# Optimization experiments

Hardware: AMD Instinct MI355X
Metric: run time of the kernel (lower is better)

Reference implementation:

```python
import jax, jax.numpy as jnp
import numpy as np

D_MODEL = 2048
N_HEADS = 16
D_HEAD = 128
INIT_RANGE = 0.02
EPSILON = -100000.0  # mask fill value from the original module


def setup_inputs() -> dict:
    key = jax.random.key(0)
    ks = jax.random.split(key, 6)
    x = jax.random.normal(ks[0], (2, 2048, D_MODEL), dtype=jnp.float32)
    W_Q = jax.random.normal(ks[1], (N_HEADS, D_MODEL, D_HEAD), dtype=jnp.float32) * INIT_RANGE
    W_K = jax.random.normal(ks[2], (N_HEADS, D_MODEL, D_HEAD), dtype=jnp.float32) * INIT_RANGE
    W_V = jax.random.normal(ks[3], (N_HEADS, D_MODEL, D_HEAD), dtype=jnp.float32) * INIT_RANGE
    W_O = jax.random.normal(ks[4], (N_HEADS, D_HEAD, D_MODEL), dtype=jnp.float32) * INIT_RANGE
    b_Q = jnp.zeros((N_HEADS, D_HEAD), dtype=jnp.float32)
    b_K = jnp.zeros((N_HEADS, D_HEAD), dtype=jnp.float32)
    b_V = jnp.zeros((N_HEADS, D_HEAD), dtype=jnp.float32)
    b_O = jnp.zeros((D_MODEL,), dtype=jnp.float32)
    return {"normalized_resid_pre": x, "W_Q": W_Q, "b_Q": b_Q, "W_K": W_K,
            "b_K": b_K, "W_V": W_V, "b_V": b_V, "W_O": W_O, "b_O": b_O}


def reference(normalized_resid_pre, W_Q, b_Q, W_K, b_K, W_V, b_V, W_O, b_O):
    x = normalized_resid_pre  # [b, s, d_model]
    # per-head projections: [b, s, h, d_head]
    q = jnp.einsum('bsd,hdk->bshk', x, W_Q) + b_Q
    k = jnp.einsum('bsd,hdk->bshk', x, W_K) + b_K
    v = jnp.einsum('bsd,hdk->bshk', x, W_V) + b_V
    # attention scores [b, h, q, k]
    scores = jnp.einsum('bqhk,bshk->bhqs', q, k) / jnp.sqrt(jnp.float32(D_HEAD))
    S = scores.shape[-1]
    causal = jnp.tril(jnp.ones((S, S), dtype=bool))  # True = keep
    scores = jnp.where(causal, scores, jnp.float32(EPSILON))
    pattern = jax.nn.softmax(scores, axis=-1)
    z = jnp.einsum('bhqs,bshk->bqhk', pattern, v)
    attn_out = jnp.einsum('bqhk,hkd->bqd', z, W_O) + b_O
    return attn_out
```

## Files before the change

### kernel.cpp

```cpp
#include <hip/hip_runtime.h>
#include <hip/hip_bf16.h>

typedef unsigned short bfu;
typedef short          bf16x8 __attribute__((ext_vector_type(8)));
typedef float          floatx4 __attribute__((ext_vector_type(4)));
typedef unsigned short bfu4 __attribute__((ext_vector_type(4)));
typedef unsigned int   u32x2 __attribute__((ext_vector_type(2)));

__device__ __forceinline__ bfu f2bf(float f) {
    __hip_bfloat16 h = __float2bfloat16(f);
    return __builtin_bit_cast(unsigned short, h);
}

__device__ __forceinline__ float ex2(float x) {
#if __has_builtin(__builtin_amdgcn_exp2f)
    return __builtin_amdgcn_exp2f(x);
#else
    return exp2f(x);
#endif
}

__device__ __forceinline__ void glds16(const bfu* g, bfu* l) {
    __builtin_amdgcn_global_load_lds(
        (const __attribute__((address_space(1))) unsigned int*)g,
        (__attribute__((address_space(3))) unsigned int*)l, 16, 0, 0);
}

#define BATCH 2
#define SEQ   2048
#define DM    2048
#define NH    16
#define DKH   128
#define SCALE  0.08838834764831845f
#define SCALEQ 0.1275174245f

__global__ __launch_bounds__(256)
void prep(const float* __restrict__ x, bfu* __restrict__ xb,
          const float* __restrict__ WQ, const float* __restrict__ WK,
          const float* __restrict__ WV,
          bfu* __restrict__ WtQ, bfu* __restrict__ WtK, bfu* __restrict__ WtV) {
    __shared__ float tile[64][65];
    const int bid = blockIdx.x;
    if (bid < 8192) {
        const int i = (bid * 256 + threadIdx.x) * 4;
        const float4 v = *(const float4*)(x + i);
        bfu4 p; p[0] = f2bf(v.x); p[1] = f2bf(v.y); p[2] = f2bf(v.z); p[3] = f2bf(v.w);
        *(bfu4*)(xb + i) = p;
        return;
    }
    const int idx = bid - 8192;
    const int gx = idx & 1, gy = (idx >> 1) & 31, gz = idx >> 6;
    const int p = gz >> 4, h = gz & 15;
    const float* src = ((p == 0) ? WQ : (p == 1) ? WK : WV) + (size_t)h * DM * DKH;
    bfu*         dst = ((p == 0) ? WtQ : (p == 1) ? WtK : WtV) + (size_t)h * DKH * DM;
    const float  s   = (p == 0) ? SCALEQ : 1.0f;
    const int r0 = gy * 64, c0 = gx * 64;
    const int t  = threadIdx.x;
    const int lr = t >> 4;
    const int lc = (t & 15) * 4;
    #pragma unroll
    for (int pp = 0; pp < 4; pp++) {
        const float4 v = *(const float4*)(src + (size_t)(r0 + pp*16 + lr) * DKH + c0 + lc);
        tile[pp*16 + lr][lc + 0] = v.x;
        tile[pp*16 + lr][lc + 1] = v.y;
        tile[pp*16 + lr][lc + 2] = v.z;
        tile[pp*16 + lr][lc + 3] = v.w;
    }
    __syncthreads();
    const int rc = t & 15, cb = t >> 4;
    #pragma unroll
    for (int pp = 0; pp < 4; pp++) {
        const int c = pp*16 + cb;
        bfu4 pk;
        #pragma unroll
        for (int j = 0; j < 4; j++) pk[j] = f2bf(tile[rc*4 + j][c] * s);
        *(bfu4*)(dst + (size_t)(c0 + c) * DM + r0 + rc*4) = pk;
    }
}

__global__ __launch_bounds__(256)
void tcvt_wo64(const float* __restrict__ WO, bfu* __restrict__ WtO) {
    __shared__ float tile[64][65];
    const int r0 = blockIdx.y * 64, c0 = blockIdx.x * 64;
    const int t  = threadIdx.x;
    const int lr = t >> 4;
    const int lc = (t & 15) * 4;
    #pragma unroll
    for (int pp = 0; pp < 4; pp++) {
        const float4 v = *(const float4*)(WO + (size_t)(r0 + pp*16 + lr) * DM + c0 + lc);
        tile[pp*16 + lr][lc + 0] = v.x;
        tile[pp*16 + lr][lc + 1] = v.y;
        tile[pp*16 + lr][lc + 2] = v.z;
        tile[pp*16 + lr][lc + 3] = v.w;
    }
    __syncthreads();
    const int rc = t & 15, cb = t >> 4;
    #pragma unroll
    for (int pp = 0; pp < 4; pp++) {
        const int c = pp*16 + cb;
        bfu4 pk;
        #pragma unroll
        for (int j = 0; j < 4; j++) pk[j] = f2bf(tile[rc*4 + j][c]);
        *(bfu4*)(WtO + (size_t)(c0 + c) * DM + r0 + rc*4) = pk;
    }
}

__device__ __forceinline__ void stg_half(const bfu* gbase, bfu* slot,
                                         int wave, int lane, int csw) {
    #pragma unroll
    for (int l = 0; l < 2; l++) {
        const int j = l * 8 + wave;
        glds16(gbase + (size_t)((j >> 1) * 16 + (lane >> 2)) * DM
                     + (j & 1) * 32 + csw,
               slot + j * 512);
    }
}

__device__ __forceinline__ void ld_b8(bf16x8 (&bv)[4][2], const bfu* slot, int rdo) {
    #pragma unroll
    for (int n = 0; n < 4; n++)
        #pragma unroll
        for (int ks = 0; ks < 2; ks++)
            bv[n][ks] = *(const bf16x8*)&slot[(n * 2 + ks) * 512 + rdo];
}

__device__ __forceinline__ void ld_a8(bf16x8 (&af)[4][2], const bfu* slot, int rdo) {
    #pragma unroll
    for (int m = 0; m < 4; m++)
        #pragma unroll
        for (int ks = 0; ks < 2; ks++)
            af[m][ks] = *(const bf16x8*)&slot[(m * 2 + ks) * 512 + rdo];
}

template<int MH, int NHALF>
__device__ __forceinline__ void mfma16(floatx4 (&acc)[8][4],
                                       const bf16x8 (&af)[4][2],
                                       const bf16x8 (&bv)[4][2]) {
    __builtin_amdgcn_s_setprio(1);
    #pragma unroll
    for (int m = 0; m < 4; m++)
        #pragma unroll
        for (int n = 0; n < 2; n++)
            #pragma unroll
            for (int ks = 0; ks < 2; ks++)
                acc[MH*4 + m][NHALF*2 + n] =
                    __builtin_amdgcn_mfma_f32_16x16x32_bf16(
                        af[m][ks], bv[NHALF*2 + n][ks],
                        acc[MH*4 + m][NHALF*2 + n], 0, 0, 0);
    __builtin_amdgcn_s_setprio(0);
}

#define BARW()                                                      \
    __builtin_amdgcn_s_barrier();                                   \
    asm volatile("s_waitcnt lgkmcnt(0)" ::: "memory");              \
    __builtin_amdgcn_sched_barrier(0)

__global__ __launch_bounds__(512, 2)
void proj_qk8(const bfu* __restrict__ xb,
              const bfu* __restrict__ WtQ, const bfu* __restrict__ WtK,
              const float* __restrict__ bQ, const float* __restrict__ bK,
              bfu* __restrict__ Qall, bfu* __restrict__ Kall) {
    __shared__ __align__(16) bfu As[2][2][8192];
    __shared__ __align__(16) bfu Bs[2][2][8192];

    const int p = blockIdx.y >> 3;
    const bfu*   Wt   = (p == 0) ? WtQ : WtK;
    const float* bias = (p == 0) ? bQ  : bK;
    const float  bscale = (p == 0) ? SCALEQ : 1.0f;

    const int tid  = threadIdx.x;
    const int lane = tid & 63;
    const int wave = tid >> 6;
    const int lrow = lane & 15;
    const int quad = lane >> 4;
    const int wr   = wave >> 2;
    const int wc   = wave & 3;
    const size_t m0 = (size_t)blockIdx.x * 256;
    const int    n0 = (int)(blockIdx.y & 7) * 256;

    const int csw = ((lane & 3) * 8) ^ ((lane & 32) ? 16 : 0);
    const int rdo = lrow * 32 + ((quad * 8) ^ ((lrow & 8) ? 16 : 0));

    const bfu* Ab = xb + m0 * DM;
    const bfu* Bb = Wt + (size_t)n0 * DM;

    floatx4 acc[8][4] = {};
    bf16x8 af[4][2], bv[4][2];

#define STAGE_A(tau, h)                                                     \
    if ((tau) < 32) stg_half(Ab + (size_t)((h) * 128) * DM + (tau) * 64,    \
                             &As[(tau) & 1][h][0], wave, lane, csw)
#define STAGE_B(tau, h)                                                     \
    if ((tau) < 32) stg_half(Bb + (size_t)((h) * 128) * DM + (tau) * 64,    \
                             &Bs[(tau) & 1][h][0], wave, lane, csw)

    STAGE_B(0, 0); STAGE_B(0, 1); STAGE_A(0, 0); STAGE_A(0, 1);
    STAGE_B(1, 0); STAGE_B(1, 1); STAGE_A(1, 0);
    asm volatile("s_waitcnt vmcnt(6)" ::: "memory");
    __builtin_amdgcn_s_barrier();

    #pragma unroll 1
    for (int i = 0; i < 16; i++) {
        const int t0 = 2 * i;
        ld_b8(bv, &Bs[0][wc >> 1][(wc & 1) * 4096], rdo);
        ld_a8(af, &As[0][wr][0], rdo);
        STAGE_A(t0 + 1, 1);
        BARW();
        mfma16<0, 0>(acc, af, bv);
        __builtin_amdgcn_s_barrier();
        STAGE_B(t0 + 2, 0);
        BARW();
        mfma16<0, 1>(acc, af, bv);
        __builtin_amdgcn_s_barrier();
        ld_a8(af, &As[0][wr][4096], rdo);
        STAGE_B(t0 + 2, 1);
        BARW();
        mfma16<1, 0>(acc, af, bv);
        __builtin_amdgcn_s_barrier();
        STAGE_A(t0 + 2, 0);
        BARW();
        mfma16<1, 1>(acc, af, bv);
        if (i == 15) asm volatile("s_waitcnt vmcnt(0)" ::: "memory");
        else         asm volatile("s_waitcnt vmcnt(6)" ::: "memory");
        __builtin_amdgcn_s_barrier();
        ld_b8(bv, &Bs[1][wc >> 1][(wc & 1) * 4096], rdo);
        ld_a8(af, &As[1][wr][0], rdo);
        STAGE_A(t0 + 2, 1);
        BARW();
        mfma16<0, 0>(acc, af, bv);
        __builtin_amdgcn_s_barrier();
        STAGE_B(t0 + 3, 0);
        BARW();
        mfma16<0, 1>(acc, af, bv);
        __builtin_amdgcn_s_barrier();
        ld_a8(af, &As[1][wr][4096], rdo);
        STAGE_B(t0 + 3, 1);
        BARW();
        mfma16<1, 0>(acc, af, bv);
        __builtin_amdgcn_s_barrier();
        STAGE_A(t0 + 3, 0);
        BARW();
        mfma16<1, 1>(acc, af, bv);
        if (i < 15) asm volatile("s_waitcnt vmcnt(6)" ::: "memory");
        __builtin_amdgcn_s_barrier();
    }
#undef STAGE_A
#undef STAGE_B

    bfu* Out = (p == 0) ? Qall : Kall;
    #pragma unroll
    for (int m = 0; m < 8; m++) {
        #pragma unroll
        for (int n = 0; n < 4; n++) {
            const int gn = n0 + wc * 64 + n * 16 + lrow;
            const float bvv = bias[gn] * bscale;
            #pragma unroll
            for (int r = 0; r < 4; r++) {
                const size_t gm = m0 + wr * 128 + m * 16 + quad * 4 + r;
                Out[gm * DM + gn] = f2bf(acc[m][n][r] + bvv);
            }
        }
    }
}

__global__ __launch_bounds__(256)
void proj_v(const bfu* __restrict__ xb, const bfu* __restrict__ WtV,
            const float* __restrict__ bV, bfu* __restrict__ Vt) {
    __shared__ bfu As[128 * 32];
    __shared__ bfu Bs[128 * 32];
    const int tid  = threadIdx.x;
    const int lane = tid & 63;
    const int wave = tid >> 6;
    const int lrow = lane & 15;
    const int quad = lane >> 4;
    const int mw = (wave & 1) * 64;
    const int nw = (wave >> 1) * 64;
    const size_t m0 = (size_t)blockIdx.x * 128;
    const size_t n0 = (size_t)blockIdx.y * 128;
    const int rowb = lane >> 2;
    const int colb = (lane & 3) * 8;

    floatx4 acc[4][4] = {};

    for (int k0 = 0; k0 < DM; k0 += 32) {
        __syncthreads();
        #pragma unroll
        for (int i = 0; i < 2; i++) {
            const int rg = wave * 2 + i;
            glds16(xb  + (m0 + rg*16 + rowb) * DM + k0 + colb, &As[rg * 512]);
            glds16(WtV + (n0 + rg*16 + rowb) * DM + k0 + colb, &Bs[rg * 512]);
        }
        __syncthreads();
        bf16x8 af[4], bfr[4];
        #pragma unroll
        for (int t = 0; t < 4; t++) {
            af[t]  = *(const bf16x8*)&As[(mw + t*16 + lrow) * 32 + quad * 8];
            bfr[t] = *(const bf16x8*)&Bs[(nw + t*16 + lrow) * 32 + quad * 8];
        }
        #pragma unroll
        for (int mt = 0; mt < 4; mt++)
            #pragma unroll
            for (int nt = 0; nt < 4; nt++)
                acc[mt][nt] = __builtin_amdgcn_mfma_f32_16x16x32_bf16(
                                  af[mt], bfr[nt], acc[mt][nt], 0, 0, 0);
    }

    #pragma unroll
    for (int mt = 0; mt < 4; mt++) {
        #pragma unroll
        for (int nt = 0; nt < 4; nt++) {
            const int nl = (int)n0 + nw + nt*16 + lrow;
            const float bvv = bV[nl];
            const size_t gm0 = m0 + mw + mt*16 + quad*4;
            const int b = (int)(gm0 >> 11), s = (int)(gm0 & 2047);
            bfu4 pk;
            #pragma unroll
            for (int r = 0; r < 4; r++) pk[r] = f2bf(acc[mt][nt][r] + bvv);
            *(bfu4*)&Vt[((size_t)(b * NH + (nl >> 7)) * DKH + (nl & 127)) * SEQ + s] = pk;
        }
    }
}

__global__ __launch_bounds__(256)
void flash_attn(const bfu* __restrict__ Q, const bfu* __restrict__ K,
                const bfu* __restrict__ Vt, bfu* __restrict__ Z) {
    __shared__ bfu Ks[4][64][32];
    __shared__ bfu Vs[2][128][32];
    __shared__ bfu Ps[4][16][72];

    const int tid  = threadIdx.x;
    const int lane = tid & 63;
    const int wave = tid >> 6;
    const int lrow = lane & 15;
    const int quad = lane >> 4;
    const int hb = blockIdx.x;
    const int h = hb & 15, b = hb >> 4;
    const int qt = 31 - blockIdx.y;
    const int q0w = qt * 64 + wave * 16;
    const int rowb = lane >> 2;
    const int csw  = ((lane & 3) * 8) ^ ((lane & 32) ? 16 : 0);
    const int rq0  = (quad * 8) ^ ((lrow & 8) ? 16 : 0);

    const bfu* Qrow = Q + (size_t)(b * SEQ + q0w + lrow) * DM + h * DKH;
    bf16x8 qf[4];
    #pragma unroll
    for (int kc = 0; kc < 4; kc++)
        qf[kc] = *(const bf16x8*)(Qrow + kc*32 + quad*8);

    floatx4 z[8] = {};
    float l_loc = 0.f;
    const int qg = q0w + lrow;

    const bfu* Kb = K + (size_t)b * SEQ * DM + h * DKH;
    const bfu* Vb = Vt + (size_t)(b * NH + h) * DKH * SEQ;
    const int ntiles = qt + 1;

    for (int it = 0; it < ntiles; it++) {
        const int s0 = it * 64;
        __syncthreads();
        #pragma unroll
        for (int i = 0; i < 8; i++) {
            const int chunk = wave * 8 + i;
            if (chunk < 16) {
                const int kc = chunk >> 2, kg = chunk & 3;
                glds16(Kb + (size_t)(s0 + kg*16 + rowb) * DM + kc*32 + csw,
                       &Ks[kc][kg*16][0]);
            } else {
                const int c2 = chunk - 16;
                const int sh = c2 >> 3, dg = c2 & 7;
                glds16(Vb + (size_t)(dg*16 + rowb) * SEQ + s0 + sh*32 + csw,
                       &Vs[sh][dg*16][0]);
            }
        }
        __syncthreads();

        floatx4 sc[4];
        __builtin_amdgcn_s_setprio(1);
        #pragma unroll
        for (int st = 0; st < 4; st++) {
            floatx4 a = {};
            #pragma unroll
            for (int kc = 0; kc < 4; kc++) {
                bf16x8 kf = *(const bf16x8*)&Ks[kc][st*16 + lrow][rq0];
                a = __builtin_amdgcn_mfma_f32_16x16x32_bf16(kf, qf[kc], a, 0, 0, 0);
            }
            sc[st] = a;
        }
        __builtin_amdgcn_s_setprio(0);

        if (it + 1 < ntiles) {
            #pragma unroll
            for (int st = 0; st < 4; st++) {
                const float p0 = ex2(sc[st][0]);
                const float p1 = ex2(sc[st][1]);
                const float p2 = ex2(sc[st][2]);
                const float p3 = ex2(sc[st][3]);
                l_loc += (p0 + p1) + (p2 + p3);
                u32x2 pk;
                pk[0] = (unsigned)f2bf(p0) | ((unsigned)f2bf(p1) << 16);
                pk[1] = (unsigned)f2bf(p2) | ((unsigned)f2bf(p3) << 16);
                *(u32x2*)&Ps[wave][lrow][st*16 + quad*4] = pk;
            }
        } else {
            #pragma unroll
            for (int st = 0; st < 4; st++) {
                const int sbase = s0 + st*16 + quad*4;
                const float p0 = (sbase + 0 <= qg) ? ex2(sc[st][0]) : 0.f;
                const float p1 = (sbase + 1 <= qg) ? ex2(sc[st][1]) : 0.f;
                const float p2 = (sbase + 2 <= qg) ? ex2(sc[st][2]) : 0.f;
                const float p3 = (sbase + 3 <= qg) ? ex2(sc[st][3]) : 0.f;
                l_loc += (p0 + p1) + (p2 + p3);
                u32x2 pk;
                pk[0] = (unsigned)f2bf(p0) | ((unsigned)f2bf(p1) << 16);
                pk[1] = (unsigned)f2bf(p2) | ((unsigned)f2bf(p3) << 16);
                *(u32x2*)&Ps[wave][lrow][st*16 + quad*4] = pk;
            }
        }

        bf16x8 pf0 = *(const bf16x8*)&Ps[wave][lrow][quad*8];
        bf16x8 pf1 = *(const bf16x8*)&Ps[wave][lrow][32 + quad*8];
        __builtin_amdgcn_s_setprio(1);
        #pragma unroll
        for (int dt = 0; dt < 8; dt++) {
            bf16x8 v0 = *(const bf16x8*)&Vs[0][dt*16 + lrow][rq0];
            z[dt] = __builtin_amdgcn_mfma_f32_16x16x32_bf16(pf0, v0, z[dt], 0, 0, 0);
            bf16x8 v1 = *(const bf16x8*)&Vs[1][dt*16 + lrow][rq0];
            z[dt] = __builtin_amdgcn_mfma_f32_16x16x32_bf16(pf1, v1, z[dt], 0, 0, 0);
        }
        __builtin_amdgcn_s_setprio(0);
    }

    float L = l_loc;
    L += __shfl_xor(L, 16);
    L += __shfl_xor(L, 32);
    float inv[4];
    #pragma unroll
    for (int r = 0; r < 4; r++)
        inv[r] = 1.0f / __shfl(L, quad*4 + r, 64);
    #pragma unroll
    for (int dt = 0; dt < 8; dt++) {
        #pragma unroll
        for (int r = 0; r < 4; r++) {
            const int qq = q0w + quad*4 + r;
            const int dk = dt*16 + lrow;
            Z[(size_t)(b * SEQ + qq) * DM + h * DKH + dk] = f2bf(z[dt][r] * inv[r]);
        }
    }
}

__global__ __launch_bounds__(256)
void out_gemm(const bfu* __restrict__ Zb, const bfu* __restrict__ WtO,
              const float* __restrict__ bO, float* out) {
    __shared__ bfu As[128 * 32];
    __shared__ bfu Bs[128 * 32];
    const int tid  = threadIdx.x;
    const int lane = tid & 63;
    const int wave = tid >> 6;
    const int lrow = lane & 15;
    const int quad = lane >> 4;
    const int mw = (wave & 1) * 64;
    const int nw = (wave >> 1) * 64;
    const size_t m0 = (size_t)blockIdx.x * 128;
    const size_t n0 = (size_t)blockIdx.y * 128;
    const int rowb = lane >> 2, colb = (lane & 3) * 8;

    floatx4 acc[4][4] = {};

    for (int k0 = 0; k0 < DM; k0 += 32) {
        __syncthreads();
        #pragma unroll
        for (int i = 0; i < 2; i++) {
            const int rg = wave * 2 + i;
            glds16(Zb  + (m0 + rg*16 + rowb) * DM + k0 + colb, &As[rg * 512]);
            glds16(WtO + (n0 + rg*16 + rowb) * DM + k0 + colb, &Bs[rg * 512]);
        }
        __syncthreads();
        bf16x8 af[4], bfr[4];
        #pragma unroll
        for (int t = 0; t < 4; t++) {
            af[t]  = *(const bf16x8*)&As[(mw + t*16 + lrow) * 32 + quad * 8];
            bfr[t] = *(const bf16x8*)&Bs[(nw + t*16 + lrow) * 32 + quad * 8];
        }
        #pragma unroll
        for (int mt = 0; mt < 4; mt++)
            #pragma unroll
            for (int nt = 0; nt < 4; nt++)
                acc[mt][nt] = __builtin_amdgcn_mfma_f32_16x16x32_bf16(
                                  af[mt], bfr[nt], acc[mt][nt], 0, 0, 0);
    }

    #pragma unroll
    for (int mt = 0; mt < 4; mt++) {
        #pragma unroll
        for (int nt = 0; nt < 4; nt++) {
            const size_t gn = n0 + nw + nt*16 + lrow;
            const float bv = bO[gn];
            #pragma unroll
            for (int r = 0; r < 4; r++) {
                const size_t gm = m0 + mw + mt*16 + quad*4 + r;
                out[gm * DM + gn] = acc[mt][nt][r] + bv;
            }
        }
    }
}

extern "C" void kernel_launch(void* const* d_in, const int* in_sizes, int n_in,
                              void* d_out, int out_size, void* d_ws, size_t ws_size,
                              hipStream_t stream) {
    const float* x  = (const float*)d_in[0];
    const float* WQ = (const float*)d_in[1];
    const float* bQ = (const float*)d_in[2];
    const float* WK = (const float*)d_in[3];
    const float* bK = (const float*)d_in[4];
    const float* WV = (const float*)d_in[5];
    const float* bV = (const float*)d_in[6];
    const float* WO = (const float*)d_in[7];
    const float* bO = (const float*)d_in[8];
    float* out = (float*)d_out;
    bfu* ws  = (bfu*)d_ws;
    bfu* dob = (bfu*)d_out;

    bfu* Qall = ws;
    bfu* Kall = Qall + 8388608;
    bfu* Vt   = Kall + 8388608;
    bfu* Zb   = Vt   + 8388608;
    bfu* WtV  = Zb;
    bfu* xb   = dob;
    bfu* WtQ  = dob + 8388608;
    bfu* WtK  = dob + 12582912;

    prep<<<11264, 256, 0, stream>>>(x, xb, WQ, WK, WV, WtQ, WtK, WtV);

    proj_qk8<<<dim3(16, 16), 512, 0, stream>>>(xb, WtQ, WtK, bQ, bK, Qall, Kall);
    proj_v<<<dim3(32, 16), 256, 0, stream>>>(xb, WtV, bV, Vt);

    flash_attn<<<dim3(32, 32), 256, 0, stream>>>(Qall, Kall, Vt, Zb);

    tcvt_wo64<<<dim3(32, 32), 256, 0, stream>>>(WO, Qall);
    out_gemm<<<dim3(32, 16), 256, 0, stream>>>(Zb, Qall, bO, out);
}
```

Before: 364.5 us.

## Double query rows per wave in flash attention to reuse K/V tiles

Each wave now handles 32 query rows (two 16-row MFMA tiles) and each block covers 128 queries, so the grid in the query dimension is halved. Each K/V tile loaded into LDS feeds twice as many MFMAs, which cuts global and LDS traffic per unit of work. Waves whose rows are fully masked for a tile skip compute with a continue after the barrier. The cost is more registers for the extra accumulators, fewer blocks, and more load imbalance from the causal mask across waves.

```diff
diff --git a/kernel.cpp b/kernel.cpp
--- a/kernel.cpp
+++ b/kernel.cpp
@@ -326,7 +326,7 @@
                 const bfu* __restrict__ Vt, bfu* __restrict__ Z) {
     __shared__ bfu Ks[4][64][32];
     __shared__ bfu Vs[2][128][32];
-    __shared__ bfu Ps[4][16][72];
+    __shared__ bfu Ps[4][32][72];
 
     const int tid  = threadIdx.x;
     const int lane = tid & 63;
@@ -335,25 +335,29 @@
     const int quad = lane >> 4;
     const int hb = blockIdx.x;
     const int h = hb & 15, b = hb >> 4;
-    const int qt = 31 - blockIdx.y;
-    const int q0w = qt * 64 + wave * 16;
+    const int qt = 15 - blockIdx.y;
+    const int q0w = qt * 128 + wave * 32;
     const int rowb = lane >> 2;
     const int csw  = ((lane & 3) * 8) ^ ((lane & 32) ? 16 : 0);
     const int rq0  = (quad * 8) ^ ((lrow & 8) ? 16 : 0);
 
-    const bfu* Qrow = Q + (size_t)(b * SEQ + q0w + lrow) * DM + h * DKH;
-    bf16x8 qf[4];
-    #pragma unroll
-    for (int kc = 0; kc < 4; kc++)
-        qf[kc] = *(const bf16x8*)(Qrow + kc*32 + quad*8);
-
-    floatx4 z[8] = {};
-    float l_loc = 0.f;
-    const int qg = q0w + lrow;
+    const bfu* Qrow0 = Q + (size_t)(b * SEQ + q0w + lrow) * DM + h * DKH;
+    const bfu* Qrow1 = Qrow0 + (size_t)16 * DM;
+    bf16x8 qf0[4], qf1[4];
+    #pragma unroll
+    for (int kc = 0; kc < 4; kc++) {
+        qf0[kc] = *(const bf16x8*)(Qrow0 + kc*32 + quad*8);
+        qf1[kc] = *(const bf16x8*)(Qrow1 + kc*32 + quad*8);
+    }
+
+    floatx4 z0[8] = {}, z1[8] = {};
+    float l0 = 0.f, l1 = 0.f;
+    const int qg0 = q0w + lrow;
+    const int qg1 = q0w + 16 + lrow;
 
     const bfu* Kb = K + (size_t)b * SEQ * DM + h * DKH;
     const bfu* Vb = Vt + (size_t)(b * NH + h) * DKH * SEQ;
-    const int ntiles = qt + 1;
+    const int ntiles = 2 * (qt + 1);
 
     for (int it = 0; it < ntiles; it++) {
         const int s0 = it * 64;
@@ -374,76 +378,106 @@
         }
         __syncthreads();
 
-        floatx4 sc[4];
+        if (s0 > q0w + 31) continue;
+
+        floatx4 sc0[4], sc1[4];
         __builtin_amdgcn_s_setprio(1);
         #pragma unroll
         for (int st = 0; st < 4; st++) {
-            floatx4 a = {};
+            floatx4 a0 = {}, a1 = {};
             #pragma unroll
             for (int kc = 0; kc < 4; kc++) {
                 bf16x8 kf = *(const bf16x8*)&Ks[kc][st*16 + lrow][rq0];
-                a = __builtin_amdgcn_mfma_f32_16x16x32_bf16(kf, qf[kc], a, 0, 0, 0);
+                a0 = __builtin_amdgcn_mfma_f32_16x16x32_bf16(kf, qf0[kc], a0, 0, 0, 0);
+                a1 = __builtin_amdgcn_mfma_f32_16x16x32_bf16(kf, qf1[kc], a1, 0, 0, 0);
             }
-            sc[st] = a;
+            sc0[st] = a0;
+            sc1[st] = a1;
         }
         __builtin_amdgcn_s_setprio(0);
 
-        if (it + 1 < ntiles) {
+        if (s0 + 64 <= q0w) {
             #pragma unroll
             for (int st = 0; st < 4; st++) {
-                const float p0 = ex2(sc[st][0]);
-                const float p1 = ex2(sc[st][1]);
-                const float p2 = ex2(sc[st][2]);
-                const float p3 = ex2(sc[st][3]);
-                l_loc += (p0 + p1) + (p2 + p3);
+                const float p0 = ex2(sc0[st][0]);
+                const float p1 = ex2(sc0[st][1]);
+                const float p2 = ex2(sc0[st][2]);
+                const float p3 = ex2(sc0[st][3]);
+                l0 += (p0 + p1) + (p2 + p3);
                 u32x2 pk;
                 pk[0] = (unsigned)f2bf(p0) | ((unsigned)f2bf(p1) << 16);
                 pk[1] = (unsigned)f2bf(p2) | ((unsigned)f2bf(p3) << 16);
                 *(u32x2*)&Ps[wave][lrow][st*16 + quad*4] = pk;
+                const float q0_ = ex2(sc1[st][0]);
+                const float q1_ = ex2(sc1[st][1]);
+                const float q2_ = ex2(sc1[st][2]);
+                const float q3_ = ex2(sc1[st][3]);
+                l1 += (q0_ + q1_) + (q2_ + q3_);
+                u32x2 qk;
+                qk[0] = (unsigned)f2bf(q0_) | ((unsigned)f2bf(q1_) << 16);
+                qk[1] = (unsigned)f2bf(q2_) | ((unsigned)f2bf(q3_) << 16);
+                *(u32x2*)&Ps[wave][16 + lrow][st*16 + quad*4] = qk;
             }
         } else {
             #pragma unroll
             for (int st = 0; st < 4; st++) {
                 const int sbase = s0 + st*16 + quad*4;
-                const float p0 = (sbase + 0 <= qg) ? ex2(sc[st][0]) : 0.f;
-                const float p1 = (sbase + 1 <= qg) ? ex2(sc[st][1]) : 0.f;
-                const float p2 = (sbase + 2 <= qg) ? ex2(sc[st][2]) : 0.f;
-                const float p3 = (sbase + 3 <= qg) ? ex2(sc[st][3]) : 0.f;
-                l_loc += (p0 + p1) + (p2 + p3);
+                const float p0 = (sbase + 0 <= qg0) ? ex2(sc0[st][0]) : 0.f;
+                const float p1 = (sbase + 1 <= qg0) ? ex2(sc0[st][1]) : 0.f;
+                const float p2 = (sbase + 2 <= qg0) ? ex2(sc0[st][2]) : 0.f;
+                const float p3 = (sbase + 3 <= qg0) ? ex2(sc0[st][3]) : 0.f;
+                l0 += (p0 + p1) + (p2 + p3);
                 u32x2 pk;
                 pk[0] = (unsigned)f2bf(p0) | ((unsigned)f2bf(p1) << 16);
                 pk[1] = (unsigned)f2bf(p2) | ((unsigned)f2bf(p3) << 16);
                 *(u32x2*)&Ps[wave][lrow][st*16 + quad*4] = pk;
+                const float q0_ = (sbase + 0 <= qg1) ? ex2(sc1[st][0]) : 0.f;
+                const float q1_ = (sbase + 1 <= qg1) ? ex2(sc1[st][1]) : 0.f;
+                const float q2_ = (sbase + 2 <= qg1) ? ex2(sc1[st][2]) : 0.f;
+                const float q3_ = (sbase + 3 <= qg1) ? ex2(sc1[st][3]) : 0.f;
+                l1 += (q0_ + q1_) + (q2_ + q3_);
+                u32x2 qk;
+                qk[0] = (unsigned)f2bf(q0_) | ((unsigned)f2bf(q1_) << 16);
+                qk[1] = (unsigned)f2bf(q2_) | ((unsigned)f2bf(q3_) << 16);
+                *(u32x2*)&Ps[wave][16 + lrow][st*16 + quad*4] = qk;
             }
         }
 
-        bf16x8 pf0 = *(const bf16x8*)&Ps[wave][lrow][quad*8];
-        bf16x8 pf1 = *(const bf16x8*)&Ps[wave][lrow][32 + quad*8];
+        bf16x8 pf00 = *(const bf16x8*)&Ps[wave][lrow][quad*8];
+        bf16x8 pf01 = *(const bf16x8*)&Ps[wave][lrow][32 + quad*8];
+        bf16x8 pf10 = *(const bf16x8*)&Ps[wave][16 + lrow][quad*8];
+        bf16x8 pf11 = *(const bf16x8*)&Ps[wave][16 + lrow][32 + quad*8];
         __builtin_amdgcn_s_setprio(1);
         #pragma unroll
         for (int dt = 0; dt < 8; dt++) {
             bf16x8 v0 = *(const bf16x8*)&Vs[0][dt*16 + lrow][rq0];
-            z[dt] = __builtin_amdgcn_mfma_f32_16x16x32_bf16(pf0, v0, z[dt], 0, 0, 0);
+            z0[dt] = __builtin_amdgcn_mfma_f32_16x16x32_bf16(pf00, v0, z0[dt], 0, 0, 0);
+            z1[dt] = __builtin_amdgcn_mfma_f32_16x16x32_bf16(pf10, v0, z1[dt], 0, 0, 0);
             bf16x8 v1 = *(const bf16x8*)&Vs[1][dt*16 + lrow][rq0];
-            z[dt] = __builtin_amdgcn_mfma_f32_16x16x32_bf16(pf1, v1, z[dt], 0, 0, 0);
+            z0[dt] = __builtin_amdgcn_mfma_f32_16x16x32_bf16(pf01, v1, z0[dt], 0, 0, 0);
+            z1[dt] = __builtin_amdgcn_mfma_f32_16x16x32_bf16(pf11, v1, z1[dt], 0, 0, 0);
         }
         __builtin_amdgcn_s_setprio(0);
     }
 
-    float L = l_loc;
-    L += __shfl_xor(L, 16);
-    L += __shfl_xor(L, 32);
-    float inv[4];
-    #pragma unroll
-    for (int r = 0; r < 4; r++)
-        inv[r] = 1.0f / __shfl(L, quad*4 + r, 64);
+    float L0 = l0, L1 = l1;
+    L0 += __shfl_xor(L0, 16);  L0 += __shfl_xor(L0, 32);
+    L1 += __shfl_xor(L1, 16);  L1 += __shfl_xor(L1, 32);
+    float inv0[4], inv1[4];
+    #pragma unroll
+    for (int r = 0; r < 4; r++) {
+        inv0[r] = 1.0f / __shfl(L0, quad*4 + r, 64);
+        inv1[r] = 1.0f / __shfl(L1, quad*4 + r, 64);
+    }
     #pragma unroll
     for (int dt = 0; dt < 8; dt++) {
         #pragma unroll
         for (int r = 0; r < 4; r++) {
-            const int qq = q0w + quad*4 + r;
             const int dk = dt*16 + lrow;
-            Z[(size_t)(b * SEQ + qq) * DM + h * DKH + dk] = f2bf(z[dt][r] * inv[r]);
+            const int qq0 = q0w + quad*4 + r;
+            Z[(size_t)(b * SEQ + qq0) * DM + h * DKH + dk] = f2bf(z0[dt][r] * inv0[r]);
+            const int qq1 = q0w + 16 + quad*4 + r;
+            Z[(size_t)(b * SEQ + qq1) * DM + h * DKH + dk] = f2bf(z1[dt][r] * inv1[r]);
         }
     }
 }
@@ -534,7 +568,7 @@
     proj_qk8<<<dim3(16, 16), 512, 0, stream>>>(xb, WtQ, WtK, bQ, bK, Qall, Kall);
     proj_v<<<dim3(32, 16), 256, 0, stream>>>(xb, WtV, bV, Vt);
 
-    flash_attn<<<dim3(32, 32), 256, 0, stream>>>(Qall, Kall, Vt, Zb);
+    flash_attn<<<dim3(32, 16), 256, 0, stream>>>(Qall, Kall, Vt, Zb);
 
     tcvt_wo64<<<dim3(32, 32), 256, 0, stream>>>(WO, Qall);
     out_gemm<<<dim3(32, 16), 256, 0, stream>>>(Zb, Qall, bO, out);
```

After: 374.6 us. 2.8% more time.
